# Optimization experiments

Measured on AMD Instinct MI355X. Metric: run time of the kernel, lower is better.

Reference implementation:

```python
import jax, jax.numpy as jnp
import numpy as np

STATE = 1024

def setup_inputs() -> dict:
    key = jax.random.key(0)
    k1, k2, k3, k4, k5 = jax.random.split(key, 5)
    B, IN, S = 4096, 1024, STATE
    stdv = 1.0 / np.sqrt(S)
    return {
        "input": jax.random.normal(k1, (B, IN), jnp.float32),
        "old_h": jax.random.normal(k2, (B, S), jnp.float32),
        "old_cell": jax.random.normal(k3, (B, S), jnp.float32),
        "weights": jax.random.uniform(k4, (4 * S, IN + S), jnp.float32, -stdv, stdv),
        "bias": jax.random.uniform(k5, (4 * S,), jnp.float32, -stdv, stdv),
    }

def reference(input, old_h, old_cell, weights, bias):
    # Fused gate GEMM: X = [input, old_h] -> [B, IN+S]; gates -> [B, 4S]
    X = jnp.concatenate([input, old_h], axis=1)
    gates = X @ weights.T + bias
    f, i, o, g = jnp.split(gates, 4, axis=1)
    f = jax.nn.sigmoid(f)
    i = jax.nn.sigmoid(i)
    o = jax.nn.sigmoid(o)
    g = jnp.tanh(g)
    new_cell = f * old_cell + i * g
    new_h = o * jnp.tanh(new_cell)
    return new_h, new_cell
```

## Files before the change

kernel.cpp:

```cpp
#include <hip/hip_runtime.h>
#include <stdint.h>

#define NB   4096
#define KD   2048
#define ND   4096
#define SD   1024

#define BM   256
#define BN   256
#define BK   64
#define NKT  (KD / BK)

using f32x4  = __attribute__((ext_vector_type(4))) float;
using bf16x8 = __attribute__((ext_vector_type(8))) short;

typedef const __attribute__((address_space(1))) uint32_t* gas_u32;
typedef __attribute__((address_space(3))) uint32_t* las_u32;

__device__ __forceinline__ unsigned short f2bf(float f) {
    union { float f; uint32_t u; } c; c.f = f;
    uint32_t u = c.u;
    uint32_t r = (u + 0x7fffu + ((u >> 16) & 1u)) >> 16;
    return (unsigned short)r;
}

__device__ __forceinline__ void async_load16(const void* gsrc, void* ldst) {
    __builtin_amdgcn_global_load_lds((gas_u32)gsrc, (las_u32)ldst, 16, 0, 0);
}

__device__ __forceinline__ float frcp(float x) { return __builtin_amdgcn_rcpf(x); }
__device__ __forceinline__ float sigm(float x) { return frcp(1.f + __expf(-x)); }
__device__ __forceinline__ float tanh_fast(float x) {
    return 1.f - 2.f * frcp(1.f + __expf(2.f * x));
}

__global__ void pack_kernel(const float* __restrict__ input,
                            const float* __restrict__ old_h,
                            const float* __restrict__ weights,
                            const float* __restrict__ bias,
                            unsigned short* __restrict__ Xb,
                            unsigned short* __restrict__ Wb,
                            float* __restrict__ biasR) {
    const int XCH = NB * (KD / 4);
    const int WCH = ND * (KD / 4);
    const int BCH = ND / 4;
    const int total = XCH + WCH + BCH;
    for (int c = blockIdx.x * blockDim.x + threadIdx.x; c < total;
         c += gridDim.x * blockDim.x) {
        if (c < XCH) {
            int b  = c >> 9;
            int k  = (c & 511) << 2;
            const float* src = (k < 1024) ? (input + (size_t)b * 1024 + k)
                                          : (old_h + (size_t)b * 1024 + (k - 1024));
            float4 v = *reinterpret_cast<const float4*>(src);
            ushort4 o;
            o.x = f2bf(v.x); o.y = f2bf(v.y); o.z = f2bf(v.z); o.w = f2bf(v.w);
            *reinterpret_cast<ushort4*>(Xb + (size_t)b * KD + k) = o;
        } else if (c < XCH + WCH) {
            int cc = c - XCH;
            int n  = cc >> 9;
            int k  = (cc & 511) << 2;
            int srow = ((n >> 4) & 3) * SD + ((n >> 6) * 16 + (n & 15));
            float4 v = *reinterpret_cast<const float4*>(weights + (size_t)srow * KD + k);
            ushort4 o;
            o.x = f2bf(v.x); o.y = f2bf(v.y); o.z = f2bf(v.z); o.w = f2bf(v.w);
            *reinterpret_cast<ushort4*>(Wb + (size_t)n * KD + k) = o;
        } else {
            int n4 = (c - XCH - WCH) << 2;
            #pragma unroll
            for (int t = 0; t < 4; ++t) {
                int n = n4 + t;
                biasR[n] = bias[((n >> 4) & 3) * SD + ((n >> 6) * 16 + (n & 15))];
            }
        }
    }
}

#define SEG(DB, AB, HALF) (((((DB) * 2 + (AB)) * 2) + (HALF)) * 8192)

#define SBAR   __builtin_amdgcn_s_barrier()
#define ASM_LGKM0  asm volatile("s_waitcnt lgkmcnt(0)" ::: "memory")
#define ASM_VMCNT2 asm volatile("s_waitcnt vmcnt(2)" ::: "memory")
#define ASM_VMCNT8 asm volatile("s_waitcnt vmcnt(8)" ::: "memory")

__launch_bounds__(512, 2)
__global__ void lstm_gemm(const unsigned short* __restrict__ Xb,
                          const unsigned short* __restrict__ Wb,
                          const float* __restrict__ biasR,
                          const float* __restrict__ old_cell,
                          float* __restrict__ new_h,
                          float* __restrict__ new_cell) {
    __shared__ unsigned short lds[65536];

    const int tid  = threadIdx.x;
    const int lane = tid & 63;
    const int wid  = tid >> 6;
    const int wm   = wid >> 2;
    const int wn   = wid & 3;
    const int l15  = lane & 15;
    const int krow = lane >> 4;

    const int wg    = blockIdx.x;
    const int swz   = (wg & 7) * 32 + (wg >> 3);
    const int mblk  = swz >> 4;
    const int nblk  = swz & 15;
    const int rbase = mblk * BM;
    const int nbase = nblk * BN;

    const int c0 = tid, c1 = tid + 512;
    const int srow0 = c0 >> 3, sk0 = ((c0 & 7) ^ (srow0 & 7)) * 8;
    const int srow1 = c1 >> 3, sk1 = ((c1 & 7) ^ (srow1 & 7)) * 8;

    f32x4  acc[8][4] = {};
    bf16x8 a[4][2];
    bf16x8 bm[2][2];
    bf16x8 ba[2][2];

#define STAGE(PTR, TB, KT, DB, AB, HALF) do {                                   \
        async_load16((PTR) + (size_t)((TB) + (HALF) * 128 + srow0) * KD +       \
                         (KT) * BK + sk0,                                       \
                     lds + SEG(DB, AB, HALF) + c0 * 8);                         \
        async_load16((PTR) + (size_t)((TB) + (HALF) * 128 + srow1) * KD +       \
                         (KT) * BK + sk1,                                       \
                     lds + SEG(DB, AB, HALF) + c1 * 8);                         \
    } while (0)

#define LOAD_A(DB, MQ) do {                                                     \
        const unsigned short* base_ = lds + SEG(DB, 0, 0) + wm * 8192;          \
        _Pragma("unroll") for (int i_ = 0; i_ < 4; ++i_)                        \
        _Pragma("unroll") for (int kk_ = 0; kk_ < 2; ++kk_) {                   \
            int r_ = (MQ) * 64 + i_ * 16 + l15;                                 \
            int s_ = kk_ * 4 + krow;                                            \
            a[i_][kk_] = *reinterpret_cast<const bf16x8*>(                      \
                base_ + r_ * 64 + ((s_ ^ (r_ & 7)) * 8));                       \
        }                                                                       \
    } while (0)

#define LOAD_B_TO(DST, DB, NQ) do {                                             \
        const unsigned short* base_ = lds + SEG(DB, 1, 0) + (wn >> 1) * 8192;   \
        _Pragma("unroll") for (int j_ = 0; j_ < 2; ++j_)                        \
        _Pragma("unroll") for (int kk_ = 0; kk_ < 2; ++kk_) {                   \
            int r_ = (wn & 1) * 64 + ((NQ) * 2 + j_) * 16 + l15;                \
            int s_ = kk_ * 4 + krow;                                            \
            DST[j_][kk_] = *reinterpret_cast<const bf16x8*>(                    \
                base_ + r_ * 64 + ((s_ ^ (r_ & 7)) * 8));                       \
        }                                                                       \
    } while (0)

#define MMA_Q(MQ, NQH, BB) do {                                                 \
        _Pragma("unroll") for (int i_ = 0; i_ < 4; ++i_)                        \
        _Pragma("unroll") for (int j_ = 0; j_ < 2; ++j_)                        \
        _Pragma("unroll") for (int kk_ = 0; kk_ < 2; ++kk_)                     \
            acc[(MQ) * 4 + i_][(NQH) * 2 + j_] =                                \
                __builtin_amdgcn_mfma_f32_16x16x32_bf16(                        \
                    a[i_][kk_], BB[j_][kk_],                                    \
                    acc[(MQ) * 4 + i_][(NQH) * 2 + j_], 0, 0, 0);               \
    } while (0)

#define PH_HEAD   ASM_LGKM0; SBAR; __builtin_amdgcn_s_setprio(1)
#define PH_HEADV  ASM_LGKM0; ASM_VMCNT2; SBAR; __builtin_amdgcn_s_setprio(1)
#define PRIO0     __builtin_amdgcn_s_setprio(0)

    STAGE(Wb, nbase, 0, 0, 1, 0);
    STAGE(Wb, nbase, 0, 0, 1, 1);
    STAGE(Xb, rbase, 0, 0, 0, 0);
    STAGE(Xb, rbase, 0, 0, 0, 1);
    STAGE(Wb, nbase, 1, 1, 1, 0);
    STAGE(Wb, nbase, 1, 1, 1, 1);
    STAGE(Xb, rbase, 1, 1, 0, 0);
    STAGE(Xb, rbase, 1, 1, 0, 1);
    ASM_VMCNT8;
    SBAR;
    LOAD_B_TO(bm, 0, 0);
    LOAD_A(0, 0);

#define KBODY(TT, BUF) do {                                                     \
        const int kt2_ = ((TT) + 2) & (NKT - 1);                                \
                                                                        \
        PH_HEAD;  MMA_Q(0, 0, bm); LOAD_B_TO(ba, BUF, 1);       PRIO0;          \
                                                                        \
        PH_HEAD;  MMA_Q(0, 1, ba); LOAD_A(BUF, 1);              PRIO0;          \
        STAGE(Wb, nbase, kt2_, BUF, 1, 0);                                      \
                                                                        \
        PH_HEADV; MMA_Q(1, 0, bm); LOAD_B_TO(bm, (BUF) ^ 1, 0); PRIO0;          \
        STAGE(Wb, nbase, kt2_, BUF, 1, 1);                                      \
        STAGE(Xb, rbase, kt2_, BUF, 0, 0);                                      \
                                                                        \
        PH_HEAD;  MMA_Q(1, 1, ba); LOAD_A((BUF) ^ 1, 0);        PRIO0;          \
        STAGE(Xb, rbase, kt2_, BUF, 0, 1);                                      \
    } while (0)

    for (int t = 0; t < NKT; t += 2) {
        KBODY(t, 0);
        KBODY(t + 1, 1);
    }

    const int s = (nblk * 4 + wn) * 16 + l15;
    float bg[4];
    #pragma unroll
    for (int jj = 0; jj < 4; ++jj)
        bg[jj] = biasR[nbase + wn * 64 + jj * 16 + l15];

    #pragma unroll
    for (int mi = 0; mi < 8; ++mi) {
        #pragma unroll
        for (int r = 0; r < 4; ++r) {
            const int row = rbase + wm * 128 + mi * 16 + krow * 4 + r;
            float fg = sigm(acc[mi][0][r] + bg[0]);
            float ig = sigm(acc[mi][1][r] + bg[1]);
            float og = sigm(acc[mi][2][r] + bg[2]);
            float gg = tanh_fast(acc[mi][3][r] + bg[3]);
            float oc = old_cell[(size_t)row * SD + s];
            float nc = fmaf(fg, oc, ig * gg);
            float nh = og * tanh_fast(nc);
            new_h[(size_t)row * SD + s]    = nh;
            new_cell[(size_t)row * SD + s] = nc;
        }
    }
}

extern "C" void kernel_launch(void* const* d_in, const int* in_sizes, int n_in,
                              void* d_out, int out_size, void* d_ws, size_t ws_size,
                              hipStream_t stream) {
    const float* input    = (const float*)d_in[0];
    const float* old_h    = (const float*)d_in[1];
    const float* old_cell = (const float*)d_in[2];
    const float* weights  = (const float*)d_in[3];
    const float* bias     = (const float*)d_in[4];

    unsigned short* Xb  = (unsigned short*)d_ws;
    unsigned short* Wb  = (unsigned short*)((char*)d_ws + (size_t)16777216);
    float*          bR  = (float*)((char*)d_ws + (size_t)33554432);

    float* out_h = (float*)d_out;
    float* out_c = out_h + (size_t)NB * SD;

    pack_kernel<<<2048, 256, 0, stream>>>(input, old_h, weights, bias, Xb, Wb, bR);
    lstm_gemm<<<(NB / BM) * (ND / BN), 512, 0, stream>>>(Xb, Wb, bR, old_cell,
                                                         out_h, out_c);
}
```

Before: 77.62 us.

## Restructure GEMM main loop into eight-phase schedule with staggered X/W prefetch

Rewrites the bf16 MFMA main loop as eight phases per pair of K tiles. Each phase issues LDS fragment reads and one global-to-LDS async stage, then waits on a barrier and runs one MMA quadrant at raised priority. X tiles are now prefetched one tile ahead and W tiles two ahead, instead of both two ahead, and vmcnt/lgkmcnt waits are relaxed to partial counts. The aim is to overlap memory traffic with matrix math more evenly. In exchange it doubles the barriers per tile and reduces prefetch distance for X, and the asm waits without memory clobbers risk reordering hazards.

```diff
diff --git a/kernel.cpp b/kernel.cpp
--- a/kernel.cpp
+++ b/kernel.cpp
@@ -79,9 +79,11 @@
 #define SEG(DB, AB, HALF) (((((DB) * 2 + (AB)) * 2) + (HALF)) * 8192)
 
 #define SBAR   __builtin_amdgcn_s_barrier()
-#define ASM_LGKM0  asm volatile("s_waitcnt lgkmcnt(0)" ::: "memory")
-#define ASM_VMCNT2 asm volatile("s_waitcnt vmcnt(2)" ::: "memory")
-#define ASM_VMCNT8 asm volatile("s_waitcnt vmcnt(8)" ::: "memory")
+#define LGKM8  asm volatile("s_waitcnt lgkmcnt(8)")
+#define LGKM0  asm volatile("s_waitcnt lgkmcnt(0)")
+#define VMC4   asm volatile("s_waitcnt vmcnt(4)" ::: "memory")
+#define PRIO1  __builtin_amdgcn_s_setprio(1)
+#define PRIO0  __builtin_amdgcn_s_setprio(0)
 
 __launch_bounds__(512, 2)
 __global__ void lstm_gemm(const unsigned short* __restrict__ Xb,
@@ -113,8 +115,8 @@
 
     f32x4  acc[8][4] = {};
     bf16x8 a[4][2];
-    bf16x8 bm[2][2];
-    bf16x8 ba[2][2];
+    bf16x8 b0[2][2];
+    bf16x8 b1[2][2];
 
 #define STAGE(PTR, TB, KT, DB, AB, HALF) do {                                   \
         async_load16((PTR) + (size_t)((TB) + (HALF) * 128 + srow0) * KD +       \
@@ -157,42 +159,57 @@
                     acc[(MQ) * 4 + i_][(NQH) * 2 + j_], 0, 0, 0);               \
     } while (0)
 
-#define PH_HEAD   ASM_LGKM0; SBAR; __builtin_amdgcn_s_setprio(1)
-#define PH_HEADV  ASM_LGKM0; ASM_VMCNT2; SBAR; __builtin_amdgcn_s_setprio(1)
-#define PRIO0     __builtin_amdgcn_s_setprio(0)
-
     STAGE(Wb, nbase, 0, 0, 1, 0);
     STAGE(Wb, nbase, 0, 0, 1, 1);
     STAGE(Xb, rbase, 0, 0, 0, 0);
     STAGE(Xb, rbase, 0, 0, 0, 1);
     STAGE(Wb, nbase, 1, 1, 1, 0);
     STAGE(Wb, nbase, 1, 1, 1, 1);
-    STAGE(Xb, rbase, 1, 1, 0, 0);
-    STAGE(Xb, rbase, 1, 1, 0, 1);
-    ASM_VMCNT8;
+    VMC4;
     SBAR;
-    LOAD_B_TO(bm, 0, 0);
-    LOAD_A(0, 0);
-
-#define KBODY(TT, BUF) do {                                                     \
+
+#define KBODY(TT) do {                                                          \
+        const int kt1_ = (TT) + 1;                                              \
         const int kt2_ = ((TT) + 2) & (NKT - 1);                                \
-                                                                        \
-        PH_HEAD;  MMA_Q(0, 0, bm); LOAD_B_TO(ba, BUF, 1);       PRIO0;          \
-                                                                        \
-        PH_HEAD;  MMA_Q(0, 1, ba); LOAD_A(BUF, 1);              PRIO0;          \
-        STAGE(Wb, nbase, kt2_, BUF, 1, 0);                                      \
-                                                                        \
-        PH_HEADV; MMA_Q(1, 0, bm); LOAD_B_TO(bm, (BUF) ^ 1, 0); PRIO0;          \
-        STAGE(Wb, nbase, kt2_, BUF, 1, 1);                                      \
-        STAGE(Xb, rbase, kt2_, BUF, 0, 0);                                      \
-                                                                        \
-        PH_HEAD;  MMA_Q(1, 1, ba); LOAD_A((BUF) ^ 1, 0);        PRIO0;          \
-        STAGE(Xb, rbase, kt2_, BUF, 0, 1);                                      \
+        const int kt3_ = ((TT) + 3) & (NKT - 1);                                \
+                                                 \
+        LOAD_A(0, 0);                                                           \
+        LOAD_B_TO(b0, 0, 0);                                                    \
+        STAGE(Xb, rbase, kt1_, 1, 0, 0);                                        \
+        LGKM8;                                                                  \
+        SBAR; LGKM0; PRIO1; MMA_Q(0, 0, b0); PRIO0; SBAR;                       \
+                                                        \
+        LOAD_B_TO(b1, 0, 1);                                                    \
+        STAGE(Xb, rbase, kt1_, 1, 0, 1);                                        \
+        SBAR; LGKM0; PRIO1; MMA_Q(0, 1, b1); PRIO0; SBAR;                       \
+                                                        \
+        LOAD_A(0, 1);                                                           \
+        STAGE(Wb, nbase, kt2_, 0, 1, 0);                                        \
+        SBAR; LGKM0; PRIO1; MMA_Q(1, 0, b0); PRIO0; SBAR;                       \
+                               \
+        STAGE(Wb, nbase, kt2_, 0, 1, 1);                                        \
+        SBAR; LGKM0; PRIO1; MMA_Q(1, 1, b1); PRIO0; VMC4; SBAR;                 \
+                                               \
+        LOAD_A(1, 0);                                                           \
+        LOAD_B_TO(b0, 1, 0);                                                    \
+        STAGE(Xb, rbase, kt2_, 0, 0, 0);                                        \
+        LGKM8;                                                                  \
+        SBAR; LGKM0; PRIO1; MMA_Q(0, 0, b0); PRIO0; SBAR;                       \
+                                                        \
+        LOAD_B_TO(b1, 1, 1);                                                    \
+        STAGE(Xb, rbase, kt2_, 0, 0, 1);                                        \
+        SBAR; LGKM0; PRIO1; MMA_Q(0, 1, b1); PRIO0; SBAR;                       \
+                                                        \
+        LOAD_A(1, 1);                                                           \
+        STAGE(Wb, nbase, kt3_, 1, 1, 0);                                        \
+        SBAR; LGKM0; PRIO1; MMA_Q(1, 0, b0); PRIO0; SBAR;                       \
+                               \
+        STAGE(Wb, nbase, kt3_, 1, 1, 1);                                        \
+        SBAR; LGKM0; PRIO1; MMA_Q(1, 1, b1); PRIO0; VMC4; SBAR;                 \
     } while (0)
 
     for (int t = 0; t < NKT; t += 2) {
-        KBODY(t, 0);
-        KBODY(t + 1, 1);
+        KBODY(t);
     }
 
     const int s = (nblk * 4 + wn) * 16 + l15;
```

Result: slower. 80.62 us (+3.9%).
